# Kernel optimization log

Hardware: AMD Instinct MI355X
Metric: run time of the kernel (lower is better)

The kernel has to match this reference:

```python
import jax, jax.numpy as jnp
import numpy as np

B, N, E = 8, 4096, 65536
FIN, OUT, T, H = 128, 128, 4, 4
C = OUT // H  # per-head channels
NEG_SLOPE = 0.2
EPS_LN = 1e-5


def setup_inputs() -> dict:
    key = jax.random.key(0)
    ks = jax.random.split(key, 10)
    x = jax.random.normal(ks[0], (B, N, FIN), dtype=jnp.float32)
    edge_index = jax.random.randint(ks[1], (B, 2, E), 0, N, dtype=jnp.int64)
    edge_type = jax.random.randint(ks[2], (B, E), 0, T, dtype=jnp.int64)
    # per-edge-type GATConv params (PyG GATConv: lin weight, att_src, att_dst, bias)
    W = jax.random.normal(ks[3], (T, FIN, H * C), dtype=jnp.float32) / np.sqrt(FIN)
    a_src = jax.random.normal(ks[4], (T, H, C), dtype=jnp.float32) / np.sqrt(C)
    a_dst = jax.random.normal(ks[5], (T, H, C), dtype=jnp.float32) / np.sqrt(C)
    bias = jnp.zeros((T, H * C), dtype=jnp.float32)
    gamma = jnp.ones((OUT,), dtype=jnp.float32)
    beta = jnp.zeros((OUT,), dtype=jnp.float32)
    return {"x": x, "edge_index": edge_index, "edge_type": edge_type,
            "W": W, "a_src": a_src, "a_dst": a_dst, "bias": bias,
            "gamma": gamma, "beta": beta}


def _gat_aggregate(h, src, dst, mask):
    """Single-graph masked GAT aggregation.
    h: [N,H,C] transformed features; src,dst: [E]; mask: [E] bool.
    Returns [N,H,C].
    """
    n = h.shape[0]
    a_s = h[src]                     # [E,H,C] source features (messages)
    # attention logits: att_src . h_src + att_dst . h_dst, done by caller via h-dot
    return a_s, n


def reference(x, edge_index, edge_type, W, a_src, a_dst, bias, gamma, beta):
    b, n, _ = x.shape
    src = edge_index[:, 0, :]  # [B,E]
    dst = edge_index[:, 1, :]

    def per_graph(e_logit, src_b, dst_b, mask_b, h_b):
        # e_logit: [E,H]; h_b: [N,H,C]
        e_m = jnp.where(mask_b[:, None], e_logit, -1e30)
        m = jax.ops.segment_max(e_m, dst_b, num_segments=n)      # [N,H]
        m = jnp.maximum(m, -1e30)
        ex = jnp.exp(e_m - m[dst_b]) * mask_b[:, None]           # [E,H]
        den = jax.ops.segment_sum(ex, dst_b, num_segments=n)     # [N,H]
        alpha = ex / (den[dst_b] + 1e-16)                        # [E,H]
        msg = alpha[:, :, None] * h_b[src_b]                     # [E,H,C]
        return jax.ops.segment_sum(msg, dst_b, num_segments=n)   # [N,H,C]

    out = jnp.zeros((b, n, H * C), dtype=x.dtype)
    for t in range(T):
        h = jnp.einsum('bnf,fo->bno', x, W[t]).reshape(b, n, H, C)
        al_s = jnp.einsum('bnhc,hc->bnh', h, a_src[t])           # [B,N,H]
        al_d = jnp.einsum('bnhc,hc->bnh', h, a_dst[t])
        e = jax.nn.leaky_relu(
            jnp.take_along_axis(al_s, src[..., None], axis=1) +
            jnp.take_along_axis(al_d, dst[..., None], axis=1),
            negative_slope=NEG_SLOPE)                            # [B,E,H]
        mask = (edge_type == t)
        agg = jax.vmap(per_graph)(e, src, dst, mask, h)          # [B,N,H,C]
        out = out + agg.reshape(b, n, H * C) + bias[t]
    # residual + LayerNorm (dropout is identity in eval)
    y = x + out
    mu = jnp.mean(y, axis=-1, keepdims=True)
    var = jnp.var(y, axis=-1, keepdims=True)
    return (y - mu) / jnp.sqrt(var + EPS_LN) * gamma + beta
```

## Files before the change

kernel.cpp:

```cpp
#include <hip/hip_runtime.h>

typedef unsigned int uint;
typedef unsigned short ushort;
typedef __attribute__((ext_vector_type(8))) short short8;
typedef __attribute__((ext_vector_type(4))) float f32x4;

#define Bb 8
#define Nn 4096
#define Ee 65536
#define Tt 4

__device__ __forceinline__ ushort bf16_rne_u(float f) {
    uint u = __float_as_uint(f);
    u += 0x7FFFu + ((u >> 16) & 1u);
    return (ushort)(u >> 16);
}

__global__ __launch_bounds__(256) void fused_a_kernel(
    const int* __restrict__ ei, const int* __restrict__ et, uint* __restrict__ count,
    const float* __restrict__ W, ushort* __restrict__ Wf,
    const float* __restrict__ bias, float* __restrict__ bias_sum)
{
    int bid = blockIdx.x;
    int tid = threadIdx.x;
    if (bid < 2048) {
        int i = bid * 256 + tid;
        int b = i >> 16;
        int e = i & (Ee - 1);
        int dst = ei[(size_t)b * 2 * Ee + Ee + e];
        int t = et[(size_t)b * Ee + e];
        atomicAdd(&count[(((uint)(b * Nn + dst)) << 2) | (uint)t], 1u);
    } else if (bid < 2080) {
        int gid = (bid - 2048) * 256 + tid;
        int t    = gid >> 11;
        int rem  = gid & 2047;
        int ks   = rem >> 9;
        int rem2 = rem & 511;
        int nt   = rem2 >> 6;
        int lane = rem2 & 63;
        int n  = nt * 16 + (lane & 15);
        int g  = lane >> 4;
        int k0 = ks * 32 + 4 * g;
        const float* Wt = W + t * 16384;
        union { uint4 q; ushort u[8]; } P;
#pragma unroll
        for (int j = 0; j < 4; ++j) P.u[j]     = bf16_rne_u(Wt[(size_t)(k0 + j) * 128 + n]);
#pragma unroll
        for (int j = 0; j < 4; ++j) P.u[4 + j] = bf16_rne_u(Wt[(size_t)(k0 + 16 + j) * 128 + n]);
        *reinterpret_cast<uint4*>(Wf + (size_t)gid * 8) = P.q;
    } else {
        if (tid < 128)
            bias_sum[tid] = bias[tid] + bias[128 + tid] + bias[256 + tid] + bias[384 + tid];
    }
}

__global__ __launch_bounds__(256, 4) void fused_b_kernel(
    const float* __restrict__ x, const ushort* __restrict__ Wf,
    const float* __restrict__ a_src, const float* __restrict__ a_dst,
    ushort* __restrict__ h, float* __restrict__ al_s, float* __restrict__ al_d,
    const uint* __restrict__ cnt, uint* __restrict__ offs, uint* __restrict__ bsum)
{
    __shared__ ushort Hst[4][1024];

    int tid = threadIdx.x;

    if (blockIdx.x >= 1024) {
        uint* ws = reinterpret_cast<uint*>(&Hst[0][0]);
        int cblk = blockIdx.x - 1024;
        int lane = tid & 63, wv = tid >> 6;
        uint4 c = reinterpret_cast<const uint4*>(cnt)[cblk * 256 + tid];
        uint tot = c.x + c.y + c.z + c.w;
        uint inc = tot;
#pragma unroll
        for (int d = 1; d < 64; d <<= 1) {
            uint tv = (uint)__shfl_up((int)inc, d);
            if (lane >= d) inc += tv;
        }
        if (lane == 63) ws[wv] = inc;
        __syncthreads();
        uint wexcl = 0;
        for (int w = 0; w < wv; ++w) wexcl += ws[w];
        uint P = wexcl + inc - tot;
        uint4 o;
        o.x = P; o.y = P + c.x; o.z = o.y + c.y; o.w = o.z + c.z;
        reinterpret_cast<uint4*>(offs)[cblk * 256 + tid] = o;
        if (tid == 255) bsum[cblk] = P + tot;
        return;
    }

    int blk    = blockIdx.x;
    int b      = blk >> 7;
    int rowblk = blk & 127;
    int w    = tid >> 6;
    int lane = tid & 63;
    int nl = lane & 15;
    int g  = lane >> 4;
    int rg  = w & 1;
    int chn = w >> 1;
    int row0 = rowblk * 32 + rg * 16;
    ushort* hw = Hst[w];

    short8 Ah[4], Al[4];
    {
        const float* xr = x + ((size_t)b * Nn + row0 + nl) * 128;
#pragma unroll
        for (int ks = 0; ks < 4; ++ks) {
            float4 fa = *reinterpret_cast<const float4*>(xr + ks * 32 + 4 * g);
            float4 fb = *reinterpret_cast<const float4*>(xr + ks * 32 + 16 + 4 * g);
            float v[8] = {fa.x, fa.y, fa.z, fa.w, fb.x, fb.y, fb.z, fb.w};
            union { short8 s; ushort u[8]; } H, L;
#pragma unroll
            for (int j = 0; j < 8; ++j) {
                ushort hi = bf16_rne_u(v[j]);
                float fh = __uint_as_float(((uint)hi) << 16);
                H.u[j] = hi;
                L.u[j] = bf16_rne_u(v[j] - fh);
            }
            Ah[ks] = H.s;
            Al[ks] = L.s;
        }
    }

    const uint4* Wfq = reinterpret_cast<const uint4*>(Wf);

    for (int t = 0; t < Tt; ++t) {
        f32x4 acc[4];
#pragma unroll
        for (int i = 0; i < 4; ++i) acc[i] = (f32x4){0.f, 0.f, 0.f, 0.f};
#pragma unroll
        for (int ks = 0; ks < 4; ++ks) {
            union { uint4 q; short8 s; } F[4];
#pragma unroll
            for (int i = 0; i < 4; ++i)
                F[i].q = Wfq[(((t * 4 + ks) * 8) + chn * 4 + i) * 64 + lane];
#pragma unroll
            for (int i = 0; i < 4; ++i) {
                acc[i] = __builtin_amdgcn_mfma_f32_16x16x32_bf16(Ah[ks], F[i].s, acc[i], 0, 0, 0);
                acc[i] = __builtin_amdgcn_mfma_f32_16x16x32_bf16(Al[ks], F[i].s, acc[i], 0, 0, 0);
            }
        }

        {
            float as[4], ad[4];
#pragma unroll
            for (int i = 0; i < 4; ++i) {
                as[i] = a_src[t * 128 + chn * 64 + i * 16 + nl];
                ad[i] = a_dst[t * 128 + chn * 64 + i * 16 + nl];
            }
#pragma unroll
            for (int ih = 0; ih < 2; ++ih) {
#pragma unroll
                for (int r = 0; r < 4; ++r) {
                    float ps = acc[2 * ih][r] * as[2 * ih] + acc[2 * ih + 1][r] * as[2 * ih + 1];
                    float pd = acc[2 * ih][r] * ad[2 * ih] + acc[2 * ih + 1][r] * ad[2 * ih + 1];
#pragma unroll
                    for (int off = 1; off < 16; off <<= 1) {
                        ps += __shfl_xor(ps, off);
                        pd += __shfl_xor(pd, off);
                    }
                    if (nl == 0) {
                        int rowg = row0 + 4 * g + r;
                        int head = 2 * chn + ih;
                        al_s[((size_t)(b * Tt + t) * Nn + rowg) * 4 + head] = ps;
                        al_d[((size_t)(b * Tt + t) * Nn + rowg) * 4 + head] = pd;
                    }
                }
            }
        }

#pragma unroll
        for (int i = 0; i < 4; ++i) {
#pragma unroll
            for (int r = 0; r < 4; ++r) {
                int rowl  = 4 * g + r;
                int colws = i * 16 + nl;
                hw[rowl * 64 + (colws ^ ((rowl & 3) << 3))] = bf16_rne_u(acc[i][r]);
            }
        }

        {
            ushort* hb = h + ((size_t)(b * Tt + t) * Nn + row0) * 128 + chn * 64;
#pragma unroll
            for (int p = 0; p < 2; ++p) {
                int task = p * 64 + lane;
                int rowl = task >> 3;
                int c8   = (task & 7) * 8;
                uint4 v = *reinterpret_cast<const uint4*>(&hw[rowl * 64 + (c8 ^ ((rowl & 3) << 3))]);
                *reinterpret_cast<uint4*>(hb + (size_t)rowl * 128 + c8) = v;
            }
        }
    }
}

__global__ __launch_bounds__(128) void scan2_kernel(
    const uint* __restrict__ bsum, uint* __restrict__ bsx)
{
    __shared__ uint w0tot;
    int tid = threadIdx.x, lane = tid & 63, wv = tid >> 6;
    uint v = bsum[tid], inc = v;
#pragma unroll
    for (int d = 1; d < 64; d <<= 1) {
        uint tv = (uint)__shfl_up((int)inc, d);
        if (lane >= d) inc += tv;
    }
    if (tid == 63) w0tot = inc;
    __syncthreads();
    uint add = (wv == 1) ? w0tot : 0u;
    bsx[tid] = add + inc - v;
}

__global__ __launch_bounds__(256) void scatter_lr_kernel(
    const int* __restrict__ ei, const int* __restrict__ et,
    const float* __restrict__ al_s, const float* __restrict__ al_d,
    const uint* __restrict__ offs, const uint* __restrict__ bsx,
    uint* __restrict__ cursor, uint* __restrict__ src_sorted, float4* __restrict__ lr_sorted)
{
    int i = blockIdx.x * 256 + threadIdx.x;
    int b = i >> 16;
    int e = i & (Ee - 1);
    int src = ei[(size_t)b * 2 * Ee + e];
    int dst = ei[(size_t)b * 2 * Ee + Ee + e];
    int t = et[(size_t)b * Ee + e];
    uint g = (((uint)(b * Nn + dst)) << 2) | (uint)t;
    uint slot = atomicAdd(&cursor[g], 1u);
    uint p = offs[g] + bsx[g >> 10] + slot;

    size_t btN = (size_t)(b * Tt + t) * Nn;
    float4 s4 = *reinterpret_cast<const float4*>(&al_s[(btN + src) * 4]);
    float4 d4 = *reinterpret_cast<const float4*>(&al_d[(btN + dst) * 4]);
    float4 lr;
    lr.x = s4.x + d4.x; lr.x = lr.x > 0.f ? lr.x : 0.2f * lr.x;
    lr.y = s4.y + d4.y; lr.y = lr.y > 0.f ? lr.y : 0.2f * lr.y;
    lr.z = s4.z + d4.z; lr.z = lr.z > 0.f ? lr.z : 0.2f * lr.z;
    lr.w = s4.w + d4.w; lr.w = lr.w > 0.f ? lr.w : 0.2f * lr.w;
    src_sorted[p] = (uint)src;
    lr_sorted[p] = lr;
}

__global__ __launch_bounds__(256) void gat_ln_kernel(
    const float* __restrict__ x, const ushort* __restrict__ h,
    const uint* __restrict__ count, const uint* __restrict__ offs, const uint* __restrict__ bsx,
    const uint* __restrict__ src_sorted, const float4* __restrict__ lr_sorted,
    const float* __restrict__ bias_sum, const float* __restrict__ gamma, const float* __restrict__ beta,
    float* __restrict__ out)
{
    __shared__ uint  su_s[16][96];
    __shared__ float ew_s[16][96 * 4];

    int tid = threadIdx.x;
    int wl   = tid >> 6;
    int lane = tid & 63;
    int ng = lane >> 4;
    int cl = lane & 15;
    int c0 = cl << 3;
    int hh = cl >> 2;
    int grp = wl * 4 + ng;
    uint*  su = su_s[grp];
    float* ew = ew_s[grp];

    int wid = blockIdx.x * 16 + grp;
    int b   = wid >> 12;
    int dst = wid & (Nn - 1);

    uint4 cnt4 = reinterpret_cast<const uint4*>(count)[wid];
    uint4 off4 = reinterpret_cast<const uint4*>(offs)[wid];
    uint base  = off4.x + bsx[((uint)wid) >> 8];
    uint D     = min(off4.w + cnt4.w - off4.x, 96u);

    for (uint i = cl; i < D; i += 16) {
        float4 l4 = lr_sorted[base + i];
        su[i] = src_sorted[base + i];
        ew[i * 4 + 0] = __expf(l4.x);
        ew[i * 4 + 1] = __expf(l4.y);
        ew[i * 4 + 2] = __expf(l4.z);
        ew[i * 4 + 3] = __expf(l4.w);
    }
    __syncthreads();

    uint rel[4] = {0u, off4.y - off4.x, off4.z - off4.x, off4.w - off4.x};
    uint ctv[4] = {cnt4.x, cnt4.y, cnt4.z, cnt4.w};

    float tot[8];
#pragma unroll
    for (int k = 0; k < 8; ++k) tot[k] = 0.f;

#pragma unroll
    for (int t = 0; t < Tt; ++t) {
        uint ct = ctv[t];
        if (!ct) continue;
        uint p0 = rel[t];
        const ushort* hs = h + (size_t)(b * Tt + t) * Nn * 128;

        float acc[8];
#pragma unroll
        for (int k = 0; k < 8; ++k) acc[k] = 0.f;
        float den = 0.f;

        for (uint j = 0; j < ct; ++j) {
            uint i = p0 + j;
            float aw = ew[i * 4 + hh];
            uint  sj = su[i];
            uint4 hv = *reinterpret_cast<const uint4*>(hs + (size_t)sj * 128 + c0);
            float f0 = __uint_as_float(hv.x << 16);
            float f1 = __uint_as_float(hv.x & 0xFFFF0000u);
            float f2 = __uint_as_float(hv.y << 16);
            float f3 = __uint_as_float(hv.y & 0xFFFF0000u);
            float f4 = __uint_as_float(hv.z << 16);
            float f5 = __uint_as_float(hv.z & 0xFFFF0000u);
            float f6 = __uint_as_float(hv.w << 16);
            float f7 = __uint_as_float(hv.w & 0xFFFF0000u);
            acc[0] += aw * f0; acc[1] += aw * f1;
            acc[2] += aw * f2; acc[3] += aw * f3;
            acc[4] += aw * f4; acc[5] += aw * f5;
            acc[6] += aw * f6; acc[7] += aw * f7;
            den += aw;
        }
        float rden = 1.f / (den + 1e-16f);
#pragma unroll
        for (int k = 0; k < 8; ++k) tot[k] += acc[k] * rden;
    }

    size_t obase = ((size_t)b * Nn + dst) * 128 + c0;
    float y[8];
    {
        float4 xa = *reinterpret_cast<const float4*>(x + obase);
        float4 xb = *reinterpret_cast<const float4*>(x + obase + 4);
        float4 ba = *reinterpret_cast<const float4*>(bias_sum + c0);
        float4 bb = *reinterpret_cast<const float4*>(bias_sum + c0 + 4);
        y[0] = xa.x + tot[0] + ba.x; y[1] = xa.y + tot[1] + ba.y;
        y[2] = xa.z + tot[2] + ba.z; y[3] = xa.w + tot[3] + ba.w;
        y[4] = xb.x + tot[4] + bb.x; y[5] = xb.y + tot[5] + bb.y;
        y[6] = xb.z + tot[6] + bb.z; y[7] = xb.w + tot[7] + bb.w;
    }

    float s = 0.f, ss = 0.f;
#pragma unroll
    for (int k = 0; k < 8; ++k) { s += y[k]; ss += y[k] * y[k]; }
#pragma unroll
    for (int off = 1; off < 16; off <<= 1) {
        s += __shfl_xor(s, off);
        ss += __shfl_xor(ss, off);
    }
    float mu = s * (1.f / 128.f);
    float var = ss * (1.f / 128.f) - mu * mu;
    float rstd = rsqrtf(var + 1e-5f);

    float4 ga = *reinterpret_cast<const float4*>(gamma + c0);
    float4 gb = *reinterpret_cast<const float4*>(gamma + c0 + 4);
    float4 ea = *reinterpret_cast<const float4*>(beta + c0);
    float4 eb = *reinterpret_cast<const float4*>(beta + c0 + 4);
    float4 o1, o2;
    o1.x = (y[0] - mu) * rstd * ga.x + ea.x;
    o1.y = (y[1] - mu) * rstd * ga.y + ea.y;
    o1.z = (y[2] - mu) * rstd * ga.z + ea.z;
    o1.w = (y[3] - mu) * rstd * ga.w + ea.w;
    o2.x = (y[4] - mu) * rstd * gb.x + eb.x;
    o2.y = (y[5] - mu) * rstd * gb.y + eb.y;
    o2.z = (y[6] - mu) * rstd * gb.z + eb.z;
    o2.w = (y[7] - mu) * rstd * gb.w + eb.w;
    *reinterpret_cast<float4*>(out + obase) = o1;
    *reinterpret_cast<float4*>(out + obase + 4) = o2;
}

extern "C" void kernel_launch(void* const* d_in, const int* in_sizes, int n_in,
                              void* d_out, int out_size, void* d_ws, size_t ws_size,
                              hipStream_t stream)
{
    const float* x     = (const float*)d_in[0];
    const int*   ei    = (const int*)d_in[1];
    const int*   et    = (const int*)d_in[2];
    const float* W     = (const float*)d_in[3];
    const float* a_src = (const float*)d_in[4];
    const float* a_dst = (const float*)d_in[5];
    const float* bias  = (const float*)d_in[6];
    const float* gamma = (const float*)d_in[7];
    const float* beta  = (const float*)d_in[8];
    float* out = (float*)d_out;

    ushort* h   = (ushort*)d_ws;
    size_t hsz  = (size_t)Bb * Tt * Nn * 128;
    float* al_s = (float*)(h + hsz);
    size_t alsz = (size_t)Bb * Tt * Nn * 4;
    float* al_d = al_s + alsz;
    uint* count  = (uint*)(al_d + alsz);
    uint* cursor = count + (size_t)Bb * Tt * Nn;
    uint* offs   = cursor + (size_t)Bb * Tt * Nn;
    uint* bsum   = offs + (size_t)Bb * Tt * Nn;
    uint* bsx    = bsum + 128;
    float* bias_sum = (float*)(bsx + 128);
    uint* src_sorted = (uint*)(bias_sum + 128);
    float4* lr_sorted = (float4*)(src_sorted + (size_t)Bb * Ee);
    ushort* Wf = (ushort*)(lr_sorted + (size_t)Bb * Ee);

    hipMemsetAsync(count, 0, (size_t)Bb * Tt * Nn * 2 * sizeof(uint), stream);

    fused_a_kernel<<<2081, 256, 0, stream>>>(ei, et, count, W, Wf, bias, bias_sum);
    fused_b_kernel<<<1152, 256, 0, stream>>>(x, Wf, a_src, a_dst, h, al_s, al_d,
                                             count, offs, bsum);
    scan2_kernel<<<1, 128, 0, stream>>>(bsum, bsx);
    scatter_lr_kernel<<<(Bb * Ee) / 256, 256, 0, stream>>>(
        ei, et, al_s, al_d, offs, bsx, cursor, src_sorted, lr_sorted);
    gat_ln_kernel<<<(Bb * Nn) / 16, 256, 0, stream>>>(
        x, h, count, offs, bsx, src_sorted, lr_sorted, bias_sum, gamma, beta, out);
}
```

Before: 181.6 us.

## Fold attention vectors into weight MFMA and inline block-sum scan into consumers

Precomputes W·a_src and W·a_dst as an extra bf16 MFMA B-fragment column tile, so the attention logits come out of one extra MFMA per k-step instead of a shuffle-reduction epilogue. It also removes the single-block scan2 kernel: each block of the scatter and aggregation kernels recomputes the 128-entry prefix over bsum in shared memory. This saves one launch and the shuffle work, at the cost of redundant tiny scans per block and the folded logits being rounded to bf16 weights (hi/lo split on the activations only).

```diff
diff --git a/kernel.cpp b/kernel.cpp
--- a/kernel.cpp
+++ b/kernel.cpp
@@ -18,7 +18,8 @@
 
 __global__ __launch_bounds__(256) void fused_a_kernel(
     const int* __restrict__ ei, const int* __restrict__ et, uint* __restrict__ count,
-    const float* __restrict__ W, ushort* __restrict__ Wf,
+    const float* __restrict__ W, const float* __restrict__ a_src,
+    const float* __restrict__ a_dst, ushort* __restrict__ Wf,
     const float* __restrict__ bias, float* __restrict__ bias_sum)
 {
     int bid = blockIdx.x;
@@ -30,24 +31,41 @@
         int dst = ei[(size_t)b * 2 * Ee + Ee + e];
         int t = et[(size_t)b * Ee + e];
         atomicAdd(&count[(((uint)(b * Nn + dst)) << 2) | (uint)t], 1u);
-    } else if (bid < 2080) {
+    } else if (bid < 2084) {
         int gid = (bid - 2048) * 256 + tid;
-        int t    = gid >> 11;
-        int rem  = gid & 2047;
-        int ks   = rem >> 9;
-        int rem2 = rem & 511;
+        int t    = gid / 2304;
+        int rem  = gid % 2304;
+        int ks   = rem / 576;
+        int rem2 = rem % 576;
         int nt   = rem2 >> 6;
         int lane = rem2 & 63;
-        int n  = nt * 16 + (lane & 15);
+        int nl = lane & 15;
         int g  = lane >> 4;
         int k0 = ks * 32 + 4 * g;
         const float* Wt = W + t * 16384;
         union { uint4 q; ushort u[8]; } P;
-#pragma unroll
-        for (int j = 0; j < 4; ++j) P.u[j]     = bf16_rne_u(Wt[(size_t)(k0 + j) * 128 + n]);
-#pragma unroll
-        for (int j = 0; j < 4; ++j) P.u[4 + j] = bf16_rne_u(Wt[(size_t)(k0 + 16 + j) * 128 + n]);
-        *reinterpret_cast<uint4*>(Wf + (size_t)gid * 8) = P.q;
+        if (nt < 8) {
+            int n = nt * 16 + nl;
+#pragma unroll
+            for (int j = 0; j < 4; ++j) P.u[j]     = bf16_rne_u(Wt[(size_t)(k0 + j) * 128 + n]);
+#pragma unroll
+            for (int j = 0; j < 4; ++j) P.u[4 + j] = bf16_rne_u(Wt[(size_t)(k0 + 16 + j) * 128 + n]);
+        } else if (nl < 8) {
+            const float* av = (nl < 4) ? a_src : a_dst;
+            const float* ah = av + t * 128 + (nl & 3) * 32;
+#pragma unroll
+            for (int j = 0; j < 8; ++j) {
+                int k = k0 + (j < 4 ? j : 12 + j);
+                const float* wr = Wt + (size_t)k * 128 + (nl & 3) * 32;
+                float s = 0.f;
+#pragma unroll 8
+                for (int c = 0; c < 32; ++c) s += wr[c] * ah[c];
+                P.u[j] = bf16_rne_u(s);
+            }
+        } else {
+            P.q = make_uint4(0u, 0u, 0u, 0u);
+        }
+        *reinterpret_cast<uint4*>(Wf + ((size_t)((t * 4 + ks) * 9 + nt) * 64 + lane) * 8) = P.q;
     } else {
         if (tid < 128)
             bias_sum[tid] = bias[tid] + bias[128 + tid] + bias[256 + tid] + bias[384 + tid];
@@ -56,7 +74,6 @@
 
 __global__ __launch_bounds__(256, 4) void fused_b_kernel(
     const float* __restrict__ x, const ushort* __restrict__ Wf,
-    const float* __restrict__ a_src, const float* __restrict__ a_dst,
     ushort* __restrict__ h, float* __restrict__ al_s, float* __restrict__ al_d,
     const uint* __restrict__ cnt, uint* __restrict__ offs, uint* __restrict__ bsum)
 {
@@ -127,45 +144,33 @@
         f32x4 acc[4];
 #pragma unroll
         for (int i = 0; i < 4; ++i) acc[i] = (f32x4){0.f, 0.f, 0.f, 0.f};
+        f32x4 acc_al = (f32x4){0.f, 0.f, 0.f, 0.f};
+
 #pragma unroll
         for (int ks = 0; ks < 4; ++ks) {
-            union { uint4 q; short8 s; } F[4];
+            union { uint4 q; short8 s; } F[4], Fa;
 #pragma unroll
             for (int i = 0; i < 4; ++i)
-                F[i].q = Wfq[(((t * 4 + ks) * 8) + chn * 4 + i) * 64 + lane];
+                F[i].q = Wfq[((t * 4 + ks) * 9 + chn * 4 + i) * 64 + lane];
+            if (w < 2)
+                Fa.q = Wfq[((t * 4 + ks) * 9 + 8) * 64 + lane];
 #pragma unroll
             for (int i = 0; i < 4; ++i) {
                 acc[i] = __builtin_amdgcn_mfma_f32_16x16x32_bf16(Ah[ks], F[i].s, acc[i], 0, 0, 0);
                 acc[i] = __builtin_amdgcn_mfma_f32_16x16x32_bf16(Al[ks], F[i].s, acc[i], 0, 0, 0);
             }
-        }
-
-        {
-            float as[4], ad[4];
-#pragma unroll
-            for (int i = 0; i < 4; ++i) {
-                as[i] = a_src[t * 128 + chn * 64 + i * 16 + nl];
-                ad[i] = a_dst[t * 128 + chn * 64 + i * 16 + nl];
-            }
-#pragma unroll
-            for (int ih = 0; ih < 2; ++ih) {
-#pragma unroll
-                for (int r = 0; r < 4; ++r) {
-                    float ps = acc[2 * ih][r] * as[2 * ih] + acc[2 * ih + 1][r] * as[2 * ih + 1];
-                    float pd = acc[2 * ih][r] * ad[2 * ih] + acc[2 * ih + 1][r] * ad[2 * ih + 1];
-#pragma unroll
-                    for (int off = 1; off < 16; off <<= 1) {
-                        ps += __shfl_xor(ps, off);
-                        pd += __shfl_xor(pd, off);
-                    }
-                    if (nl == 0) {
-                        int rowg = row0 + 4 * g + r;
-                        int head = 2 * chn + ih;
-                        al_s[((size_t)(b * Tt + t) * Nn + rowg) * 4 + head] = ps;
-                        al_d[((size_t)(b * Tt + t) * Nn + rowg) * 4 + head] = pd;
-                    }
-                }
-            }
+            if (w < 2) {
+                acc_al = __builtin_amdgcn_mfma_f32_16x16x32_bf16(Ah[ks], Fa.s, acc_al, 0, 0, 0);
+                acc_al = __builtin_amdgcn_mfma_f32_16x16x32_bf16(Al[ks], Fa.s, acc_al, 0, 0, 0);
+            }
+        }
+
+        if (w < 2 && nl < 8) {
+            int head = nl & 3;
+            float* ap = (nl < 4 ? al_s : al_d)
+                      + ((size_t)(b * Tt + t) * Nn + row0 + 4 * g) * 4 + head;
+#pragma unroll
+            for (int r = 0; r < 4; ++r) ap[4 * r] = acc_al[r];
         }
 
 #pragma unroll
@@ -192,30 +197,29 @@
     }
 }
 
-__global__ __launch_bounds__(128) void scan2_kernel(
-    const uint* __restrict__ bsum, uint* __restrict__ bsx)
-{
-    __shared__ uint w0tot;
-    int tid = threadIdx.x, lane = tid & 63, wv = tid >> 6;
-    uint v = bsum[tid], inc = v;
-#pragma unroll
-    for (int d = 1; d < 64; d <<= 1) {
-        uint tv = (uint)__shfl_up((int)inc, d);
-        if (lane >= d) inc += tv;
-    }
-    if (tid == 63) w0tot = inc;
-    __syncthreads();
-    uint add = (wv == 1) ? w0tot : 0u;
-    bsx[tid] = add + inc - v;
-}
-
 __global__ __launch_bounds__(256) void scatter_lr_kernel(
     const int* __restrict__ ei, const int* __restrict__ et,
     const float* __restrict__ al_s, const float* __restrict__ al_d,
-    const uint* __restrict__ offs, const uint* __restrict__ bsx,
+    const uint* __restrict__ offs, const uint* __restrict__ bsum,
     uint* __restrict__ cursor, uint* __restrict__ src_sorted, float4* __restrict__ lr_sorted)
 {
-    int i = blockIdx.x * 256 + threadIdx.x;
+    __shared__ uint bsx_l[128];
+    int tid = threadIdx.x;
+    if (tid < 64) {
+        uint v0 = bsum[2 * tid], v1 = bsum[2 * tid + 1];
+        uint s = v0 + v1, inc = s;
+#pragma unroll
+        for (int d = 1; d < 64; d <<= 1) {
+            uint tv = (uint)__shfl_up((int)inc, d);
+            if (tid >= d) inc += tv;
+        }
+        uint excl = inc - s;
+        bsx_l[2 * tid] = excl;
+        bsx_l[2 * tid + 1] = excl + v0;
+    }
+    __syncthreads();
+
+    int i = blockIdx.x * 256 + tid;
     int b = i >> 16;
     int e = i & (Ee - 1);
     int src = ei[(size_t)b * 2 * Ee + e];
@@ -223,7 +227,7 @@
     int t = et[(size_t)b * Ee + e];
     uint g = (((uint)(b * Nn + dst)) << 2) | (uint)t;
     uint slot = atomicAdd(&cursor[g], 1u);
-    uint p = offs[g] + bsx[g >> 10] + slot;
+    uint p = offs[g] + bsx_l[g >> 10] + slot;
 
     size_t btN = (size_t)(b * Tt + t) * Nn;
     float4 s4 = *reinterpret_cast<const float4*>(&al_s[(btN + src) * 4]);
@@ -239,15 +243,30 @@
 
 __global__ __launch_bounds__(256) void gat_ln_kernel(
     const float* __restrict__ x, const ushort* __restrict__ h,
-    const uint* __restrict__ count, const uint* __restrict__ offs, const uint* __restrict__ bsx,
+    const uint* __restrict__ count, const uint* __restrict__ offs, const uint* __restrict__ bsum,
     const uint* __restrict__ src_sorted, const float4* __restrict__ lr_sorted,
     const float* __restrict__ bias_sum, const float* __restrict__ gamma, const float* __restrict__ beta,
     float* __restrict__ out)
 {
     __shared__ uint  su_s[16][96];
     __shared__ float ew_s[16][96 * 4];
+    __shared__ uint  bsx_l[128];
 
     int tid = threadIdx.x;
+    if (tid < 64) {
+        uint v0 = bsum[2 * tid], v1 = bsum[2 * tid + 1];
+        uint s = v0 + v1, inc = s;
+#pragma unroll
+        for (int d = 1; d < 64; d <<= 1) {
+            uint tv = (uint)__shfl_up((int)inc, d);
+            if (tid >= d) inc += tv;
+        }
+        uint excl = inc - s;
+        bsx_l[2 * tid] = excl;
+        bsx_l[2 * tid + 1] = excl + v0;
+    }
+    __syncthreads();
+
     int wl   = tid >> 6;
     int lane = tid & 63;
     int ng = lane >> 4;
@@ -264,7 +283,7 @@
 
     uint4 cnt4 = reinterpret_cast<const uint4*>(count)[wid];
     uint4 off4 = reinterpret_cast<const uint4*>(offs)[wid];
-    uint base  = off4.x + bsx[((uint)wid) >> 8];
+    uint base  = off4.x + bsx_l[((uint)wid) >> 8];
     uint D     = min(off4.w + cnt4.w - off4.x, 96u);
 
     for (uint i = cl; i < D; i += 16) {
@@ -386,20 +405,17 @@
     uint* cursor = count + (size_t)Bb * Tt * Nn;
     uint* offs   = cursor + (size_t)Bb * Tt * Nn;
     uint* bsum   = offs + (size_t)Bb * Tt * Nn;
-    uint* bsx    = bsum + 128;
-    float* bias_sum = (float*)(bsx + 128);
+    float* bias_sum = (float*)(bsum + 128);
     uint* src_sorted = (uint*)(bias_sum + 128);
     float4* lr_sorted = (float4*)(src_sorted + (size_t)Bb * Ee);
     ushort* Wf = (ushort*)(lr_sorted + (size_t)Bb * Ee);
 
     hipMemsetAsync(count, 0, (size_t)Bb * Tt * Nn * 2 * sizeof(uint), stream);
 
-    fused_a_kernel<<<2081, 256, 0, stream>>>(ei, et, count, W, Wf, bias, bias_sum);
-    fused_b_kernel<<<1152, 256, 0, stream>>>(x, Wf, a_src, a_dst, h, al_s, al_d,
-                                             count, offs, bsum);
-    scan2_kernel<<<1, 128, 0, stream>>>(bsum, bsx);
+    fused_a_kernel<<<2085, 256, 0, stream>>>(ei, et, count, W, a_src, a_dst, Wf, bias, bias_sum);
+    fused_b_kernel<<<1152, 256, 0, stream>>>(x, Wf, h, al_s, al_d, count, offs, bsum);
     scatter_lr_kernel<<<(Bb * Ee) / 256, 256, 0, stream>>>(
-        ei, et, al_s, al_d, offs, bsx, cursor, src_sorted, lr_sorted);
+        ei, et, al_s, al_d, offs, bsum, cursor, src_sorted, lr_sorted);
     gat_ln_kernel<<<(Bb * Nn) / 16, 256, 0, stream>>>(
-        x, h, count, offs, bsx, src_sorted, lr_sorted, bias_sum, gamma, beta, out);
-}
+        x, h, count, offs, bsum, src_sorted, lr_sorted, bias_sum, gamma, beta, out);
+}
```

Result: no change. 180.1 us (-0.9%).
